# Kernel tuning notes

Hardware: AMD Instinct MI355X
Metric: run time of the kernel (lower is better)

## Reference

```python
import jax, jax.numpy as jnp
import numpy as np
import math

K_HISTORY = 32  # sliding-window length over GRU hidden states


def rotate_half(x):
    half = x.shape[-1] // 2
    return jnp.concatenate([-x[..., half:], x[..., :half]], axis=-1)


def setup_inputs() -> dict:
    key = jax.random.key(0)
    ks = jax.random.split(key, 8)
    B, MB, IN = 8, 512, 1024          # batch, max_bin, input_size (gru_hidden_size)
    EMB, H, KVH, HD, BS = 1024, 16, 4, 64, 16  # embed_dim, heads, kv_heads, head_dim, bin_size
    h = jax.random.normal(ks[0], (B, MB, IN), jnp.float32)
    # RoPE tables: rotate-half layout, theta repeated over both halves
    pos = jnp.arange(MB, dtype=jnp.float32)
    inv_freq = 1.0 / (10000.0 ** (jnp.arange(0, HD, 2, dtype=jnp.float32) / HD))
    theta = pos[:, None] * inv_freq[None, :]            # (MB, HD/2)
    theta = jnp.concatenate([theta, theta], axis=-1)    # (MB, HD)
    freqs_cos = jnp.cos(theta)
    freqs_sin = jnp.sin(theta)
    s = 0.02
    Wq = jax.random.normal(ks[1], (EMB, H * HD), jnp.float32) * s
    Wk = jax.random.normal(ks[2], (IN, KVH * HD), jnp.float32) * s
    Wv = jax.random.normal(ks[3], (IN, KVH * HD), jnp.float32) * s
    Wo = jax.random.normal(ks[4], (H * HD, EMB), jnp.float32) * s
    output_queries = jax.random.normal(ks[5], (BS, EMB), jnp.float32)
    Wr = jax.random.normal(ks[6], (EMB, 2), jnp.float32) * s
    br = jnp.zeros((2,), jnp.float32)
    return {"h": h, "freqs_cos": freqs_cos, "freqs_sin": freqs_sin,
            "Wq": Wq, "Wk": Wk, "Wv": Wv, "Wo": Wo,
            "output_queries": output_queries, "Wr": Wr, "br": br}


def reference(h, freqs_cos, freqs_sin, Wq, Wk, Wv, Wo, output_queries, Wr, br):
    B, MB, IN = h.shape
    HD = freqs_cos.shape[1]
    H = Wq.shape[1] // HD
    KVH = Wk.shape[1] // HD
    n_rep = H // KVH
    BS = output_queries.shape[0]
    K = K_HISTORY

    # sliding windows over bins: window t covers h[t-K+1 : t+1] (zero left-pad)
    h_padded = jnp.concatenate([jnp.zeros((B, K - 1, IN), h.dtype), h], axis=1)
    idx = jnp.arange(MB)[:, None] + jnp.arange(K)[None, :]   # (MB, K)
    h_win = h_padded[:, idx, :]                              # (B, MB, K, IN)

    k = (h_win @ Wk).reshape(B, MB, K, KVH, HD)
    v = (h_win @ Wv).reshape(B, MB, K, KVH, HD)

    # queries: shared learned output queries, identical across batch & bins
    q = (output_queries @ Wq).reshape(BS, H, HD)             # (BS, H, HD)
    # RoPE on Q only (is_decoder=True) at within-bin offsets 0..BS-1
    offs = jnp.arange(BS)
    cos = freqs_cos[offs][:, None, :]                        # (BS, 1, HD)
    sin = freqs_sin[offs][:, None, :]
    q = q * cos + rotate_half(q) * sin                       # (BS, H, HD)

    # GQA: repeat_interleave KV heads to H heads
    k = jnp.repeat(k, n_rep, axis=3)                         # (B, MB, K, H, HD)
    v = jnp.repeat(v, n_rep, axis=3)

    scores = jnp.einsum("qhd,bmkhd->bmhqk", q, k) / math.sqrt(HD)
    attn = jax.nn.softmax(scores, axis=-1)                   # (B, MB, H, BS, K)
    attn_out = jnp.einsum("bmhqk,bmkhd->bmqhd", attn, v)
    attn_out = attn_out.reshape(B, MB, BS, H * HD)

    z = attn_out @ Wo                                        # (B, MB, BS, EMB)
    vel = z @ Wr + br                                        # (B, MB, BS, 2)
    return vel.reshape(B, MB * BS, 2)
```

## Files before the change

kernel.cpp:

```cpp
#include <hip/hip_runtime.h>


typedef __attribute__((ext_vector_type(8))) short v8s;
typedef __attribute__((ext_vector_type(4))) float v4f;

#define OFF_WOR  0u
#define OFF_QR   2048u
#define OFF_WTH  18432u
#define OFF_WTL  182272u
#define OFF_S0   346112u
#define OFF_VW0  2574336u
#define OFF_AH   2852864u
#define SROW 544

__device__ __forceinline__ void split_bf16(float a, unsigned short& h, unsigned short& l) {
    const unsigned u = __float_as_uint(a);
    h = (unsigned short)(u >> 16);
    const float r = a - __uint_as_float(u & 0xFFFF0000u);
    unsigned v = __float_as_uint(r);
    v += 0x7FFFu + ((v >> 16) & 1u);
    l = (unsigned short)(v >> 16);
}

__device__ __forceinline__ unsigned short bf16_rne(float a) {
    unsigned u = __float_as_uint(a);
    u += 0x7FFFu + ((u >> 16) & 1u);
    return (unsigned short)(u >> 16);
}

__device__ __forceinline__ size_t pidx(int j, int i) {
    return (size_t)(j >> 4) * 16384 + (size_t)((i >> 5)) * 512
         + (size_t)(((i >> 3) & 3) * 128 + (j & 15) * 8 + (i & 7));
}

__global__ __launch_bounds__(256) void kP(
    const float* __restrict__ oq, const float* __restrict__ Wq,
    const float* __restrict__ fc, const float* __restrict__ fs,
    const float* __restrict__ Wo, const float* __restrict__ Wr,
    const float* __restrict__ hsrc,
    float* __restrict__ qr, float* __restrict__ Wor,
    float* __restrict__ S0, float* __restrict__ VW0,
    unsigned short* __restrict__ Ahg)
{
    __shared__ float sm[2048];
    __shared__ unsigned short Hs[16][520];
    const int b = blockIdx.x, t = threadIdx.x;
    if (b < 256) {
        const int q = b >> 4, h = b & 15;
        #pragma unroll
        for (int j = 0; j < 4; ++j) sm[t + 256 * j] = oq[q * 1024 + t + 256 * j];
        __syncthreads();
        const int w = t >> 6, lane = t & 63;
        const float* wq = Wq + (size_t)(w * 256) * 1024 + h * 64 + lane;
        const float* os = sm + w * 256;
        float acc = 0.f;
        #pragma unroll 16
        for (int e = 0; e < 256; ++e) acc = fmaf(os[e], wq[(size_t)e * 1024], acc);
        sm[1024 + w * 64 + lane] = acc;
        __syncthreads();
        if (t < 64) {
            const int d = t, p = d ^ 32;
            const float a1 = sm[1024 + d] + sm[1088 + d] + sm[1152 + d] + sm[1216 + d];
            const float a2 = sm[1024 + p] + sm[1088 + p] + sm[1152 + p] + sm[1216 + p];
            const float c = fc[q * 64 + d], s = fs[q * 64 + d];
            const float rh = (d < 32) ? -a2 : a2;
            qr[q * 1024 + h * 64 + d] = fmaf(a1, c, rh * s);
        }
        return;
    }
    if (b < 512) {
        #pragma unroll
        for (int j = 0; j < 8; ++j) sm[t + 256 * j] = Wr[t + 256 * j];
        __syncthreads();
        const int i = (b - 256) * 4 + (t >> 6);
        const int lane = t & 63;
        float a0 = 0.f, a1 = 0.f;
        const float* wo = Wo + (size_t)i * 1024 + lane;
        #pragma unroll
        for (int j = 0; j < 16; ++j) {
            const float w = wo[j * 64];
            const int e = lane + j * 64;
            a0 = fmaf(w, sm[2 * e], a0);
            a1 = fmaf(w, sm[2 * e + 1], a1);
        }
        #pragma unroll
        for (int w = 1; w < 64; w <<= 1) {
            a0 += __shfl_xor(a0, w, 64);
            a1 += __shfl_xor(a1, w, 64);
        }
        if (lane == 0) { Wor[i * 2] = a0; Wor[i * 2 + 1] = a1; }
        return;
    }
    if (b < 1024) {
        const int b2 = b - 512;
        const int mb = b2 >> 1, kseg = b2 & 1;
        const int w = t >> 6, lane = t & 63;
        #pragma unroll
        for (int i = 0; i < 4; ++i) {
            const int r = i * 4 + w;
            const float* src = hsrc + (size_t)(mb * 16 + r) * 1024 + kseg * 512 + lane * 8;
            const float4 x0 = *(const float4*)src;
            const float4 x1 = *(const float4*)(src + 4);
            const float af[8] = {x0.x, x0.y, x0.z, x0.w, x1.x, x1.y, x1.z, x1.w};
            v8s hv;
            #pragma unroll
            for (int j = 0; j < 8; ++j) hv[j] = (short)bf16_rne(af[j]);
            *(v8s*)&Hs[r][lane * 8] = hv;
        }
        __syncthreads();
        unsigned short* dh = Ahg + (size_t)mb * 16384 + kseg * 8192;
        const int l16 = lane & 15, quad = lane >> 4;
        #pragma unroll
        for (int i = 0; i < 4; ++i) {
            const int kc = (i * 4 + w) * 32 + quad * 8;
            const v8s hv = *(const v8s*)&Hs[l16][kc];
            *(v8s*)(dh + i * 2048 + t * 8) = hv;
        }
        return;
    }
    const int idx = (b - 1024) * 256 + t;
    const float4 z = make_float4(0.f, 0.f, 0.f, 0.f);
    if (idx < 16384)  *(float4*)(S0  + (size_t)(idx >> 3) * SROW + (idx & 7) * 4) = z;
    else              *(float4*)(VW0 + (size_t)((idx - 16384) >> 3) * SROW + (idx & 7) * 4) = z;
}

__global__ __launch_bounds__(256) void kW(
    const float* __restrict__ Wk, const float* __restrict__ Wv,
    const float* __restrict__ qr, const float* __restrict__ Wor,
    unsigned short* __restrict__ Wth, unsigned short* __restrict__ Wtl)
{
    __shared__ float As[16 * 68];
    __shared__ float Bt[72 * 68];
    const int b = blockIdx.x, t = threadIdx.x;
    const int g = b & 3, i0 = (b >> 2) * 16;
    #pragma unroll
    for (int jj = 0; jj < 16; ++jj) {
        const int i2 = t + 256 * jj;
        const int d = i2 & 63, col = i2 >> 6;
        Bt[col * 68 + d] = qr[(col >> 2) * 1024 + (g * 4 + (col & 3)) * 64 + d];
    }
    #pragma unroll
    for (int jj = 0; jj < 2; ++jj) {
        const int i2 = t + 256 * jj;
        const int d = i2 & 63, vc = i2 >> 6;
        Bt[(64 + vc) * 68 + d] = Wor[((g * 4 + (vc >> 1)) * 64 + d) * 2 + (vc & 1)];
    }
    {
        const int i = t >> 4, dc = (t & 15) * 4;
        *(float4*)&As[i * 68 + dc] = *(const float4*)(Wk + (size_t)(i0 + i) * 256 + g * 64 + dc);
    }
    __syncthreads();
    const int jc = t & 63, iq = t >> 6;
    {
        float o4[4] = {0.f, 0.f, 0.f, 0.f};
        #pragma unroll
        for (int dc = 0; dc < 16; ++dc) {
            const float4 bv = *(const float4*)&Bt[jc * 68 + dc * 4];
            #pragma unroll
            for (int r = 0; r < 4; ++r) {
                const float4 av = *(const float4*)&As[(iq * 4 + r) * 68 + dc * 4];
                o4[r] = fmaf(av.x, bv.x, o4[r]);
                o4[r] = fmaf(av.y, bv.y, o4[r]);
                o4[r] = fmaf(av.z, bv.z, o4[r]);
                o4[r] = fmaf(av.w, bv.w, o4[r]);
            }
        }
        const int j = (jc >> 2) * 16 + g * 4 + (jc & 3);
        #pragma unroll
        for (int r = 0; r < 4; ++r) {
            unsigned short hh, ll;
            split_bf16(o4[r] * 0.125f, hh, ll);
            const size_t o = pidx(j, i0 + iq * 4 + r);
            Wth[o] = hh;
            Wtl[o] = ll;
        }
    }
    __syncthreads();
    {
        const int i = t >> 4, dc = (t & 15) * 4;
        *(float4*)&As[i * 68 + dc] = *(const float4*)(Wv + (size_t)(i0 + i) * 256 + g * 64 + dc);
    }
    __syncthreads();
    if (t < 128) {
        const int il = t >> 3, vc = t & 7;
        float acc = 0.f;
        #pragma unroll
        for (int dc = 0; dc < 16; ++dc) {
            const float4 av = *(const float4*)&As[il * 68 + dc * 4];
            const float4 bv = *(const float4*)&Bt[(64 + vc) * 68 + dc * 4];
            acc = fmaf(av.x, bv.x, acc);
            acc = fmaf(av.y, bv.y, acc);
            acc = fmaf(av.z, bv.z, acc);
            acc = fmaf(av.w, bv.w, acc);
        }
        const int j = 256 + (g * 4 + (vc >> 1)) * 2 + (vc & 1);
        unsigned short hh, ll;
        split_bf16(acc, hh, ll);
        const size_t o = pidx(j, i0 + il);
        Wth[o] = hh;
        Wtl[o] = ll;
    }
}

__global__ __launch_bounds__(256, 2) void k2(
    const unsigned short* __restrict__ Ahg,
    const unsigned short* __restrict__ Wth, const unsigned short* __restrict__ Wtl,
    float* __restrict__ S0, float* __restrict__ VW0)
{
    __shared__ float red[4][64][52];
    const int m0 = blockIdx.x * 64;
    const int by = blockIdx.y;
    const int t = threadIdx.x;
    const int w = t >> 6, lane = t & 63;
    const int l16 = lane & 15, quad = lane >> 4;

    const size_t abase = (size_t)blockIdx.x * 4 * 16384 + (size_t)w * 8 * 512 + lane * 8;
    const size_t bbase = (size_t)by * 3 * 16384 + (size_t)w * 8 * 512 + lane * 8;
    const unsigned short* pah = Ahg + abase;
    const unsigned short* pbh = Wth + bbase;
    const unsigned short* pbl = Wtl + bbase;

    v4f acc[4][3];
    #pragma unroll
    for (int i = 0; i < 4; ++i)
        #pragma unroll
        for (int j = 0; j < 3; ++j) acc[i][j] = (v4f)(0.f);

    v8s fah[2][4], fbh[2][3], fbl[2][3];
    #pragma unroll
    for (int s = 0; s < 4; ++s)
        fah[0][s] = *(const v8s*)(pah + s * 16384);
    #pragma unroll
    for (int s = 0; s < 3; ++s) {
        fbh[0][s] = *(const v8s*)(pbh + s * 16384);
        fbl[0][s] = *(const v8s*)(pbl + s * 16384);
    }
    #pragma unroll 8
    for (int it = 0; it < 8; ++it) {
        const int cur = it & 1, nxt = cur ^ 1;
        if (it < 7) {
            const int ko = (it + 1) * 512;
            #pragma unroll
            for (int s = 0; s < 4; ++s)
                fah[nxt][s] = *(const v8s*)(pah + s * 16384 + ko);
            #pragma unroll
            for (int s = 0; s < 3; ++s) {
                fbh[nxt][s] = *(const v8s*)(pbh + s * 16384 + ko);
                fbl[nxt][s] = *(const v8s*)(pbl + s * 16384 + ko);
            }
        }
        __builtin_amdgcn_s_setprio(1);
        #pragma unroll
        for (int ms = 0; ms < 4; ++ms)
            #pragma unroll
            for (int ns = 0; ns < 3; ++ns) {
                acc[ms][ns] = __builtin_amdgcn_mfma_f32_16x16x32_bf16(fah[cur][ms], fbl[cur][ns], acc[ms][ns], 0, 0, 0);
                acc[ms][ns] = __builtin_amdgcn_mfma_f32_16x16x32_bf16(fah[cur][ms], fbh[cur][ns], acc[ms][ns], 0, 0, 0);
            }
        __builtin_amdgcn_s_setprio(0);
    }

    #pragma unroll
    for (int ms = 0; ms < 4; ++ms)
        #pragma unroll
        for (int ns = 0; ns < 3; ++ns)
            *(v4f*)&red[w][lane][(ms * 3 + ns) * 4] = acc[ms][ns];
    __syncthreads();
    #pragma unroll
    for (int ns = 0; ns < 3; ++ns) {
        const int j = by * 48 + ns * 16 + l16;
        const int fo = (w * 3 + ns) * 4;
        const v4f s0 = *(const v4f*)&red[0][lane][fo];
        const v4f s1 = *(const v4f*)&red[1][lane][fo];
        const v4f s2 = *(const v4f*)&red[2][lane][fo];
        const v4f s3 = *(const v4f*)&red[3][lane][fo];
        const v4f sv = s0 + s1 + s2 + s3;
        const int m = m0 + w * 16 + quad * 4;
        const int bb = m >> 9, tt = m & 511;
        float* dst = (j < 256)
            ? S0  + (size_t)((bb * 16 + (j >> 4)) * 16 + (j & 15)) * SROW + 32 + tt
            : VW0 + (size_t)(bb * 32 + (j - 256)) * SROW + 32 + tt;
        *(float4*)dst = make_float4(sv[0], sv[1], sv[2], sv[3]);
    }
}

__global__ __launch_bounds__(256) void k3(
    const float* __restrict__ S, const float* __restrict__ VW,
    const float* __restrict__ brp, float* __restrict__ out)
{
    __shared__ float Es[16 * 164];
    __shared__ float EVs[32 * 164];
    const int b = blockIdx.x, q = blockIdx.y, qt = blockIdx.z;
    const int tbase = qt * 128;
    const int t = threadIdx.x;
    for (int idx = t; idx < 640; idx += 256) {
        const int h = idx / 40, g = idx - h * 40;
        const size_t off = (size_t)((b * 16 + q) * 16 + h) * SROW + tbase + g * 4;
        const float4 a = *(const float4*)(S + off);
        float4 e;
        e.x = __expf(a.x); e.y = __expf(a.y);
        e.z = __expf(a.z); e.w = __expf(a.w);
        *(float4*)(Es + h * 164 + g * 4) = e;
    }
    __syncthreads();
    for (int idx = t; idx < 1280; idx += 256) {
        const int hc = idx / 40, g = idx - hc * 40;
        const size_t off = (size_t)(b * 32 + hc) * SROW + tbase + g * 4;
        const float4 v0 = *(const float4*)(VW + off);
        const float4 e = *(const float4*)(Es + (hc >> 1) * 164 + g * 4);
        float4 rr;
        rr.x = e.x * v0.x; rr.y = e.y * v0.y;
        rr.z = e.z * v0.z; rr.w = e.w * v0.w;
        *(float4*)(EVs + hc * 164 + g * 4) = rr;
    }
    __syncthreads();
    const int h = t & 15, mg = t >> 4;
    const float* ep = Es + h * 164 + mg * 8;
    const float* e0 = EVs + (2 * h) * 164 + mg * 8;
    const float* e1 = EVs + (2 * h + 1) * 164 + mg * 8;
    float den = 0.f, n0s = 0.f, n1s = 0.f;
    #pragma unroll
    for (int s = 0; s < 32; ++s) {
        const int ss = 1 + ((s + 2 * h) & 31);
        den += ep[ss]; n0s += e0[ss]; n1s += e1[ss];
    }
    const float br0 = brp[0], br1 = brp[1];
    #pragma unroll
    for (int u = 0; u < 8; ++u) {
        const float inv = __builtin_amdgcn_rcpf(den);
        float c0 = n0s * inv, c1 = n1s * inv;
        #pragma unroll
        for (int w = 1; w < 16; w <<= 1) {
            c0 += __shfl_xor(c0, w, 64);
            c1 += __shfl_xor(c1, w, 64);
        }
        if (h == 0) {
            const int m = tbase + mg * 8 + u;
            float* o = out + (size_t)((b * 512 + m) * 16 + q) * 2;
            o[0] = c0 + br0;
            o[1] = c1 + br1;
        }
        if (u < 7) {
            den += ep[33 + u] - ep[1 + u];
            n0s += e0[33 + u] - e0[1 + u];
            n1s += e1[33 + u] - e1[1 + u];
        }
    }
}

extern "C" void kernel_launch(void* const* d_in, const int* in_sizes, int n_in,
                              void* d_out, int out_size, void* d_ws, size_t ws_size,
                              hipStream_t stream)
{
    (void)in_sizes; (void)n_in; (void)out_size; (void)ws_size;
    const float* h  = (const float*)d_in[0];
    const float* fc = (const float*)d_in[1];
    const float* fs = (const float*)d_in[2];
    const float* Wq = (const float*)d_in[3];
    const float* Wk = (const float*)d_in[4];
    const float* Wv = (const float*)d_in[5];
    const float* Wo = (const float*)d_in[6];
    const float* oq = (const float*)d_in[7];
    const float* Wr = (const float*)d_in[8];
    const float* br = (const float*)d_in[9];
    float* ws = (float*)d_ws;
    float* Wor  = ws + OFF_WOR;
    float* qr   = ws + OFF_QR;
    unsigned short* Wth = (unsigned short*)(ws + OFF_WTH);
    unsigned short* Wtl = (unsigned short*)(ws + OFF_WTL);
    float* S0   = ws + OFF_S0;
    float* VW0  = ws + OFF_VW0;
    unsigned short* Ahg = (unsigned short*)(ws + OFF_AH);
    float* out = (float*)d_out;

    hipLaunchKernelGGL(kP, dim3(1096), dim3(256), 0, stream,
                       oq, Wq, fc, fs, Wo, Wr, h, qr, Wor, S0, VW0, Ahg);
    hipLaunchKernelGGL(kW, dim3(256), dim3(256), 0, stream, Wk, Wv, qr, Wor, Wth, Wtl);
    hipLaunchKernelGGL(k2, dim3(64, 6), dim3(256), 0, stream, Ahg, Wth, Wtl, S0, VW0);
    hipLaunchKernelGGL(k3, dim3(8, 16, 4), dim3(256), 0, stream, S0, VW0, br, out);
}
```

Before: 113.6 us.

## Fuse weight-transform into GEMM kernel with atomic counter barrier, drop padding zeroing

Merges the kW weight-fold kernel into the k2 MFMA GEMM kernel. The first 256 blocks compute the folded bf16 weights, then bump a global atomic counter, and every block spin-waits on that counter before loading the B operand. It also drops the zero-padded leading 32 columns of the S/VW buffers and the kP blocks that zeroed them. k3 now substitutes exp=1 and zero values for the padded window positions in the first tile. This removes one launch and the zeroing traffic, but it depends on all 256 producer blocks being resident alongside the spinning ones, which risks deadlock or stalls.

```diff
diff --git a/kernel.cpp b/kernel.cpp
--- a/kernel.cpp
+++ b/kernel.cpp
@@ -10,8 +10,9 @@
 #define OFF_WTL  182272u
 #define OFF_S0   346112u
 #define OFF_VW0  2574336u
+#define OFF_CTR  2705408u
 #define OFF_AH   2852864u
-#define SROW 544
+#define SROW 512
 
 __device__ __forceinline__ void split_bf16(float a, unsigned short& h, unsigned short& l) {
     const unsigned u = __float_as_uint(a);
@@ -39,13 +40,13 @@
     const float* __restrict__ Wo, const float* __restrict__ Wr,
     const float* __restrict__ hsrc,
     float* __restrict__ qr, float* __restrict__ Wor,
-    float* __restrict__ S0, float* __restrict__ VW0,
-    unsigned short* __restrict__ Ahg)
+    unsigned short* __restrict__ Ahg, unsigned int* __restrict__ ctrp)
 {
     __shared__ float sm[2048];
     __shared__ unsigned short Hs[16][520];
     const int b = blockIdx.x, t = threadIdx.x;
     if (b < 256) {
+        if (b == 0 && t == 0) ctrp[0] = 0u;
         const int q = b >> 4, h = b & 15;
         #pragma unroll
         for (int j = 0; j < 4; ++j) sm[t + 256 * j] = oq[q * 1024 + t + 256 * j];
@@ -91,130 +92,125 @@
         if (lane == 0) { Wor[i * 2] = a0; Wor[i * 2 + 1] = a1; }
         return;
     }
-    if (b < 1024) {
-        const int b2 = b - 512;
-        const int mb = b2 >> 1, kseg = b2 & 1;
-        const int w = t >> 6, lane = t & 63;
-        #pragma unroll
-        for (int i = 0; i < 4; ++i) {
-            const int r = i * 4 + w;
-            const float* src = hsrc + (size_t)(mb * 16 + r) * 1024 + kseg * 512 + lane * 8;
-            const float4 x0 = *(const float4*)src;
-            const float4 x1 = *(const float4*)(src + 4);
-            const float af[8] = {x0.x, x0.y, x0.z, x0.w, x1.x, x1.y, x1.z, x1.w};
-            v8s hv;
-            #pragma unroll
-            for (int j = 0; j < 8; ++j) hv[j] = (short)bf16_rne(af[j]);
-            *(v8s*)&Hs[r][lane * 8] = hv;
-        }
-        __syncthreads();
-        unsigned short* dh = Ahg + (size_t)mb * 16384 + kseg * 8192;
-        const int l16 = lane & 15, quad = lane >> 4;
-        #pragma unroll
-        for (int i = 0; i < 4; ++i) {
-            const int kc = (i * 4 + w) * 32 + quad * 8;
-            const v8s hv = *(const v8s*)&Hs[l16][kc];
-            *(v8s*)(dh + i * 2048 + t * 8) = hv;
-        }
-        return;
-    }
-    const int idx = (b - 1024) * 256 + t;
-    const float4 z = make_float4(0.f, 0.f, 0.f, 0.f);
-    if (idx < 16384)  *(float4*)(S0  + (size_t)(idx >> 3) * SROW + (idx & 7) * 4) = z;
-    else              *(float4*)(VW0 + (size_t)((idx - 16384) >> 3) * SROW + (idx & 7) * 4) = z;
-}
-
-__global__ __launch_bounds__(256) void kW(
+    const int b2 = b - 512;
+    const int mb = b2 >> 1, kseg = b2 & 1;
+    const int w = t >> 6, lane = t & 63;
+    #pragma unroll
+    for (int i = 0; i < 4; ++i) {
+        const int r = i * 4 + w;
+        const float* src = hsrc + (size_t)(mb * 16 + r) * 1024 + kseg * 512 + lane * 8;
+        const float4 x0 = *(const float4*)src;
+        const float4 x1 = *(const float4*)(src + 4);
+        const float af[8] = {x0.x, x0.y, x0.z, x0.w, x1.x, x1.y, x1.z, x1.w};
+        v8s hv;
+        #pragma unroll
+        for (int j = 0; j < 8; ++j) hv[j] = (short)bf16_rne(af[j]);
+        *(v8s*)&Hs[r][lane * 8] = hv;
+    }
+    __syncthreads();
+    unsigned short* dh = Ahg + (size_t)mb * 16384 + kseg * 8192;
+    const int l16 = lane & 15, quad = lane >> 4;
+    #pragma unroll
+    for (int i = 0; i < 4; ++i) {
+        const int kc = (i * 4 + w) * 32 + quad * 8;
+        const v8s hv = *(const v8s*)&Hs[l16][kc];
+        *(v8s*)(dh + i * 2048 + t * 8) = hv;
+    }
+}
+
+__global__ __launch_bounds__(256, 2) void kW2(
     const float* __restrict__ Wk, const float* __restrict__ Wv,
     const float* __restrict__ qr, const float* __restrict__ Wor,
-    unsigned short* __restrict__ Wth, unsigned short* __restrict__ Wtl)
+    const unsigned short* __restrict__ Ahg,
+    unsigned short* __restrict__ Wth, unsigned short* __restrict__ Wtl,
+    float* __restrict__ S0, float* __restrict__ VW0,
+    unsigned int* __restrict__ ctrp)
 {
-    __shared__ float As[16 * 68];
-    __shared__ float Bt[72 * 68];
-    const int b = blockIdx.x, t = threadIdx.x;
-    const int g = b & 3, i0 = (b >> 2) * 16;
-    #pragma unroll
-    for (int jj = 0; jj < 16; ++jj) {
-        const int i2 = t + 256 * jj;
-        const int d = i2 & 63, col = i2 >> 6;
-        Bt[col * 68 + d] = qr[(col >> 2) * 1024 + (g * 4 + (col & 3)) * 64 + d];
-    }
-    #pragma unroll
-    for (int jj = 0; jj < 2; ++jj) {
-        const int i2 = t + 256 * jj;
-        const int d = i2 & 63, vc = i2 >> 6;
-        Bt[(64 + vc) * 68 + d] = Wor[((g * 4 + (vc >> 1)) * 64 + d) * 2 + (vc & 1)];
-    }
-    {
-        const int i = t >> 4, dc = (t & 15) * 4;
-        *(float4*)&As[i * 68 + dc] = *(const float4*)(Wk + (size_t)(i0 + i) * 256 + g * 64 + dc);
-    }
-    __syncthreads();
-    const int jc = t & 63, iq = t >> 6;
-    {
-        float o4[4] = {0.f, 0.f, 0.f, 0.f};
-        #pragma unroll
-        for (int dc = 0; dc < 16; ++dc) {
-            const float4 bv = *(const float4*)&Bt[jc * 68 + dc * 4];
+    __shared__ __align__(16) char smraw[53248];
+    const int bx = blockIdx.x, by = blockIdx.y;
+    const int bid = by * 64 + bx;
+    const int t = threadIdx.x;
+
+    if (bid < 256) {
+        float* As = (float*)smraw;
+        float* Bt = As + 16 * 68;
+        const int g = bid & 3, i0 = (bid >> 2) * 16;
+        #pragma unroll
+        for (int jj = 0; jj < 16; ++jj) {
+            const int i2 = t + 256 * jj;
+            const int d = i2 & 63, col = i2 >> 6;
+            Bt[col * 68 + d] = qr[(col >> 2) * 1024 + (g * 4 + (col & 3)) * 64 + d];
+        }
+        #pragma unroll
+        for (int jj = 0; jj < 2; ++jj) {
+            const int i2 = t + 256 * jj;
+            const int d = i2 & 63, vc = i2 >> 6;
+            Bt[(64 + vc) * 68 + d] = Wor[((g * 4 + (vc >> 1)) * 64 + d) * 2 + (vc & 1)];
+        }
+        {
+            const int i = t >> 4, dc = (t & 15) * 4;
+            *(float4*)&As[i * 68 + dc] = *(const float4*)(Wk + (size_t)(i0 + i) * 256 + g * 64 + dc);
+        }
+        __syncthreads();
+        const int jc = t & 63, iq = t >> 6;
+        {
+            float o4[4] = {0.f, 0.f, 0.f, 0.f};
+            #pragma unroll
+            for (int dc = 0; dc < 16; ++dc) {
+                const float4 bv = *(const float4*)&Bt[jc * 68 + dc * 4];
+                #pragma unroll
+                for (int r = 0; r < 4; ++r) {
+                    const float4 av = *(const float4*)&As[(iq * 4 + r) * 68 + dc * 4];
+                    o4[r] = fmaf(av.x, bv.x, o4[r]);
+                    o4[r] = fmaf(av.y, bv.y, o4[r]);
+                    o4[r] = fmaf(av.z, bv.z, o4[r]);
+                    o4[r] = fmaf(av.w, bv.w, o4[r]);
+                }
+            }
+            const int j = (jc >> 2) * 16 + g * 4 + (jc & 3);
             #pragma unroll
             for (int r = 0; r < 4; ++r) {
-                const float4 av = *(const float4*)&As[(iq * 4 + r) * 68 + dc * 4];
-                o4[r] = fmaf(av.x, bv.x, o4[r]);
-                o4[r] = fmaf(av.y, bv.y, o4[r]);
-                o4[r] = fmaf(av.z, bv.z, o4[r]);
-                o4[r] = fmaf(av.w, bv.w, o4[r]);
-            }
-        }
-        const int j = (jc >> 2) * 16 + g * 4 + (jc & 3);
-        #pragma unroll
-        for (int r = 0; r < 4; ++r) {
+                unsigned short hh, ll;
+                split_bf16(o4[r] * 0.125f, hh, ll);
+                const size_t o = pidx(j, i0 + iq * 4 + r);
+                Wth[o] = hh;
+                Wtl[o] = ll;
+            }
+        }
+        __syncthreads();
+        {
+            const int i = t >> 4, dc = (t & 15) * 4;
+            *(float4*)&As[i * 68 + dc] = *(const float4*)(Wv + (size_t)(i0 + i) * 256 + g * 64 + dc);
+        }
+        __syncthreads();
+        if (t < 128) {
+            const int il = t >> 3, vc = t & 7;
+            float acc = 0.f;
+            #pragma unroll
+            for (int dc = 0; dc < 16; ++dc) {
+                const float4 av = *(const float4*)&As[il * 68 + dc * 4];
+                const float4 bv = *(const float4*)&Bt[(64 + vc) * 68 + dc * 4];
+                acc = fmaf(av.x, bv.x, acc);
+                acc = fmaf(av.y, bv.y, acc);
+                acc = fmaf(av.z, bv.z, acc);
+                acc = fmaf(av.w, bv.w, acc);
+            }
+            const int j = 256 + (g * 4 + (vc >> 1)) * 2 + (vc & 1);
             unsigned short hh, ll;
-            split_bf16(o4[r] * 0.125f, hh, ll);
-            const size_t o = pidx(j, i0 + iq * 4 + r);
+            split_bf16(acc, hh, ll);
+            const size_t o = pidx(j, i0 + il);
             Wth[o] = hh;
             Wtl[o] = ll;
         }
-    }
-    __syncthreads();
-    {
-        const int i = t >> 4, dc = (t & 15) * 4;
-        *(float4*)&As[i * 68 + dc] = *(const float4*)(Wv + (size_t)(i0 + i) * 256 + g * 64 + dc);
-    }
-    __syncthreads();
-    if (t < 128) {
-        const int il = t >> 3, vc = t & 7;
-        float acc = 0.f;
-        #pragma unroll
-        for (int dc = 0; dc < 16; ++dc) {
-            const float4 av = *(const float4*)&As[il * 68 + dc * 4];
-            const float4 bv = *(const float4*)&Bt[(64 + vc) * 68 + dc * 4];
-            acc = fmaf(av.x, bv.x, acc);
-            acc = fmaf(av.y, bv.y, acc);
-            acc = fmaf(av.z, bv.z, acc);
-            acc = fmaf(av.w, bv.w, acc);
-        }
-        const int j = 256 + (g * 4 + (vc >> 1)) * 2 + (vc & 1);
-        unsigned short hh, ll;
-        split_bf16(acc, hh, ll);
-        const size_t o = pidx(j, i0 + il);
-        Wth[o] = hh;
-        Wtl[o] = ll;
-    }
-}
-
-__global__ __launch_bounds__(256, 2) void k2(
-    const unsigned short* __restrict__ Ahg,
-    const unsigned short* __restrict__ Wth, const unsigned short* __restrict__ Wtl,
-    float* __restrict__ S0, float* __restrict__ VW0)
-{
-    __shared__ float red[4][64][52];
-    const int m0 = blockIdx.x * 64;
-    const int by = blockIdx.y;
-    const int t = threadIdx.x;
+        __threadfence();
+        __syncthreads();
+        if (t == 0) atomicAdd(ctrp, 1u);
+    }
+
+    const int m0 = bx * 64;
     const int w = t >> 6, lane = t & 63;
     const int l16 = lane & 15, quad = lane >> 4;
-
-    const size_t abase = (size_t)blockIdx.x * 4 * 16384 + (size_t)w * 8 * 512 + lane * 8;
+    const size_t abase = (size_t)bx * 4 * 16384 + (size_t)w * 8 * 512 + lane * 8;
     const size_t bbase = (size_t)by * 3 * 16384 + (size_t)w * 8 * 512 + lane * 8;
     const unsigned short* pah = Ahg + abase;
     const unsigned short* pbh = Wth + bbase;
@@ -230,6 +226,13 @@
     #pragma unroll
     for (int s = 0; s < 4; ++s)
         fah[0][s] = *(const v8s*)(pah + s * 16384);
+
+    if (t == 0) {
+        while (atomicAdd(ctrp, 0u) < 256u) __builtin_amdgcn_s_sleep(1);
+    }
+    __syncthreads();
+    __threadfence();
+
     #pragma unroll
     for (int s = 0; s < 3; ++s) {
         fbh[0][s] = *(const v8s*)(pbh + s * 16384);
@@ -260,6 +263,7 @@
         __builtin_amdgcn_s_setprio(0);
     }
 
+    float (*red)[64][52] = (float (*)[64][52])smraw;
     #pragma unroll
     for (int ms = 0; ms < 4; ++ms)
         #pragma unroll
@@ -278,8 +282,8 @@
         const int m = m0 + w * 16 + quad * 4;
         const int bb = m >> 9, tt = m & 511;
         float* dst = (j < 256)
-            ? S0  + (size_t)((bb * 16 + (j >> 4)) * 16 + (j & 15)) * SROW + 32 + tt
-            : VW0 + (size_t)(bb * 32 + (j - 256)) * SROW + 32 + tt;
+            ? S0  + (size_t)((bb * 16 + (j >> 4)) * 16 + (j & 15)) * SROW + tt
+            : VW0 + (size_t)(bb * 32 + (j - 256)) * SROW + tt;
         *(float4*)dst = make_float4(sv[0], sv[1], sv[2], sv[3]);
     }
 }
@@ -293,24 +297,33 @@
     const int b = blockIdx.x, q = blockIdx.y, qt = blockIdx.z;
     const int tbase = qt * 128;
     const int t = threadIdx.x;
+    const bool lead = (qt == 0);
     for (int idx = t; idx < 640; idx += 256) {
         const int h = idx / 40, g = idx - h * 40;
-        const size_t off = (size_t)((b * 16 + q) * 16 + h) * SROW + tbase + g * 4;
-        const float4 a = *(const float4*)(S + off);
         float4 e;
-        e.x = __expf(a.x); e.y = __expf(a.y);
-        e.z = __expf(a.z); e.w = __expf(a.w);
+        if (lead && g < 8) {
+            e = make_float4(1.f, 1.f, 1.f, 1.f);
+        } else {
+            const size_t off = (size_t)((b * 16 + q) * 16 + h) * SROW + tbase + g * 4 - 32;
+            const float4 a = *(const float4*)(S + off);
+            e.x = __expf(a.x); e.y = __expf(a.y);
+            e.z = __expf(a.z); e.w = __expf(a.w);
+        }
         *(float4*)(Es + h * 164 + g * 4) = e;
     }
     __syncthreads();
     for (int idx = t; idx < 1280; idx += 256) {
         const int hc = idx / 40, g = idx - hc * 40;
-        const size_t off = (size_t)(b * 32 + hc) * SROW + tbase + g * 4;
-        const float4 v0 = *(const float4*)(VW + off);
-        const float4 e = *(const float4*)(Es + (hc >> 1) * 164 + g * 4);
         float4 rr;
-        rr.x = e.x * v0.x; rr.y = e.y * v0.y;
-        rr.z = e.z * v0.z; rr.w = e.w * v0.w;
+        if (lead && g < 8) {
+            rr = make_float4(0.f, 0.f, 0.f, 0.f);
+        } else {
+            const size_t off = (size_t)(b * 32 + hc) * SROW + tbase + g * 4 - 32;
+            const float4 v0 = *(const float4*)(VW + off);
+            const float4 e = *(const float4*)(Es + (hc >> 1) * 164 + g * 4);
+            rr.x = e.x * v0.x; rr.y = e.y * v0.y;
+            rr.z = e.z * v0.z; rr.w = e.w * v0.w;
+        }
         *(float4*)(EVs + hc * 164 + g * 4) = rr;
     }
     __syncthreads();
@@ -370,12 +383,13 @@
     unsigned short* Wtl = (unsigned short*)(ws + OFF_WTL);
     float* S0   = ws + OFF_S0;
     float* VW0  = ws + OFF_VW0;
+    unsigned int* ctr = (unsigned int*)(ws + OFF_CTR);
     unsigned short* Ahg = (unsigned short*)(ws + OFF_AH);
     float* out = (float*)d_out;
 
-    hipLaunchKernelGGL(kP, dim3(1096), dim3(256), 0, stream,
-                       oq, Wq, fc, fs, Wo, Wr, h, qr, Wor, S0, VW0, Ahg);
-    hipLaunchKernelGGL(kW, dim3(256), dim3(256), 0, stream, Wk, Wv, qr, Wor, Wth, Wtl);
-    hipLaunchKernelGGL(k2, dim3(64, 6), dim3(256), 0, stream, Ahg, Wth, Wtl, S0, VW0);
+    hipLaunchKernelGGL(kP, dim3(1024), dim3(256), 0, stream,
+                       oq, Wq, fc, fs, Wo, Wr, h, qr, Wor, Ahg, ctr);
+    hipLaunchKernelGGL(kW2, dim3(64, 6), dim3(256), 0, stream,
+                       Wk, Wv, qr, Wor, Ahg, Wth, Wtl, S0, VW0, ctr);
     hipLaunchKernelGGL(k3, dim3(8, 16, 4), dim3(256), 0, stream, S0, VW0, br, out);
 }
```

After: 162.8 us. 1.43x slower.
